# Kernel tuning notes

Measured on AMD Instinct MI355X. Metric: run time of the kernel, lower is better.

The kernel has to match this reference:

```python
import jax, jax.numpy as jnp
import numpy as np
from jax import lax

B, C, L = 32, 384, 3136
H_IMG = 56  # sqrt(L)
HEADS = 12
DH = C // HEADS
BN_EPS = 1e-5
ADD_EPS = 1e-12


def _branch(maps, dwk, g, b, pww, pwb, stride):
    # depthwise 3x3 conv, padding=1, no bias
    y = lax.conv_general_dilated(
        maps, dwk, window_strides=(stride, stride), padding=((1, 1), (1, 1)),
        dimension_numbers=("NCHW", "HWIO", "NCHW"), feature_group_count=C)
    # BatchNorm2d (training-mode batch stats, biased variance)
    mu = y.mean(axis=(0, 2, 3), keepdims=True)
    var = y.var(axis=(0, 2, 3), keepdims=True)
    y = (y - mu) * lax.rsqrt(var + BN_EPS)
    y = y * g[None, :, None, None] + b[None, :, None, None]
    # pointwise 1x1 conv with bias
    y = jnp.einsum("oc,bchw->bohw", pww, y) + pwb[None, :, None, None]
    return jax.nn.gelu(y, approximate=False)


def setup_inputs() -> dict:
    key = jax.random.key(0)
    ks = jax.random.split(key, 8)
    x = jax.random.normal(ks[0], (B, C, L), dtype=jnp.float32)
    dw_k = jax.random.normal(ks[1], (3, 3, 3, 1, C), dtype=jnp.float32) * 0.1  # [branch,kh,kw,1,C]
    bn2_g = jnp.ones((3, C), dtype=jnp.float32)
    bn2_b = jnp.zeros((3, C), dtype=jnp.float32)
    pw_w = jax.random.normal(ks[2], (3, C, C), dtype=jnp.float32) * (1.0 / np.sqrt(C))
    pw_b = jnp.zeros((3, C), dtype=jnp.float32)
    add_w = jnp.ones((2,), dtype=jnp.float32)
    bn1_g = jnp.ones((C,), dtype=jnp.float32)
    bn1_b = jnp.zeros((C,), dtype=jnp.float32)
    return {"x": x, "dw_k": dw_k, "bn2_g": bn2_g, "bn2_b": bn2_b,
            "pw_w": pw_w, "pw_b": pw_b, "add_w": add_w,
            "bn1_g": bn1_g, "bn1_b": bn1_b}


def reference(x, dw_k, bn2_g, bn2_b, pw_w, pw_b, add_w, bn1_g, bn1_b):
    b, c, l = x.shape
    maps = x.reshape(b, c, H_IMG, H_IMG)
    strides = (1, 2, 2)
    q, k, v = (_branch(maps, dw_k[i], bn2_g[i], bn2_b[i], pw_w[i], pw_b[i], strides[i])
               for i in range(3))
    # flatten spatial -> tokens: [B, Ltok, C] then split heads [B, Ltok, H, DH]
    def tok(t):
        bb, cc, hh, ww = t.shape
        return t.reshape(bb, cc, hh * ww).transpose(0, 2, 1).reshape(bb, hh * ww, HEADS, DH)
    qh, kh, vh = tok(q), tok(k), tok(v)
    qs = jax.nn.softmax(qh, axis=-1)      # softmax over per-head feature dim
    ks_ = jax.nn.softmax(kh, axis=1)      # softmax over k tokens
    kv = jnp.einsum("bkhd,bkhe->bhde", ks_, vh)      # [B, H, DH, DH]
    att = jnp.einsum("bqhd,bhde->bqhe", qs, kv)      # [B, Lq, H, DH]
    # per-head transpose(1,2) then cat along channels (head-major)
    att = att.transpose(0, 2, 3, 1).reshape(b, c, l)  # [B, C, L]
    # weighted residual add
    w = jax.nn.relu(add_w)
    wt = w / (w.sum() + ADD_EPS)
    y = wt[0] * att + wt[1] * x
    # BatchNorm1d over channels (training-mode batch stats)
    mu = y.mean(axis=(0, 2), keepdims=True)
    var = y.var(axis=(0, 2), keepdims=True)
    y = (y - mu) * lax.rsqrt(var + BN_EPS)
    return y * bn1_g[None, :, None] + bn1_b[None, :, None]
```

## Files before the change

kernel.cpp:

```cpp
#include <hip/hip_runtime.h>

typedef unsigned short u16;
typedef unsigned int u32;

#define NB 32
#define NC 384
#define NH 12
#define DHD 32
#define HI 56
#define LQ 3136
#define HO 28
#define LK 784

typedef _Float16 half8 __attribute__((ext_vector_type(8)));
typedef float f32x4 __attribute__((ext_vector_type(4)));

__device__ __forceinline__ u16 f2h(float f) {
  f = fminf(fmaxf(f, -60000.f), 60000.f);
  union { _Float16 h; u16 u; } v; v.h = (_Float16)f; return v.u;
}
__device__ __forceinline__ float h2f(u16 u) {
  union { u16 u; _Float16 h; } v; v.u = u; return (float)v.h;
}
__device__ __forceinline__ float gelu(float x) {
  return 0.5f * x * (1.0f + erff(x * 0.70710678118654752440f));
}

__global__ __launch_bounds__(256) void k_dwconv(
    const float* __restrict__ x, const float* __restrict__ dwk,
    u16* __restrict__ cq, u16* __restrict__ ck, u16* __restrict__ cv,
    float* __restrict__ stats2)
{
  const int c = blockIdx.x, b = blockIdx.y, t = threadIdx.x;
  __shared__ float pl[LQ];
  __shared__ float ker[32];
  __shared__ float redw[24];
  const float* xp = x + ((size_t)(b * NC + c)) * LQ;
  for (int i = t; i < LQ / 4; i += 256)
    ((float4*)pl)[i] = ((const float4*)xp)[i];
  if (t < 27) ker[t] = dwk[t * NC + c];
  __syncthreads();
  float s0 = 0, s1 = 0, s2 = 0, s3 = 0, s4 = 0, s5 = 0;
  u16* oq = cq + ((size_t)(b * NC + c)) * LQ;
  for (int p = t; p < LQ; p += 256) {
    const int h = p / HI, w = p - h * HI;
    float a = 0.f;
#pragma unroll
    for (int kh = 0; kh < 3; kh++) {
      const int hh = h + kh - 1;
      if (hh < 0 || hh >= HI) continue;
#pragma unroll
      for (int kw = 0; kw < 3; kw++) {
        const int ww = w + kw - 1;
        if (ww < 0 || ww >= HI) continue;
        a += ker[kh * 3 + kw] * pl[hh * HI + ww];
      }
    }
    const u16 rq = f2h(a);
    oq[p] = rq;
    const float ar = h2f(rq);
    s0 += ar; s1 += ar * ar;
  }
  u16* ok = ck + ((size_t)(b * NC + c)) * LK;
  u16* ov = cv + ((size_t)(b * NC + c)) * LK;
  for (int p = t; p < LK; p += 256) {
    const int h = p / HO, w = p - h * HO;
    float ak = 0.f, av = 0.f;
#pragma unroll
    for (int kh = 0; kh < 3; kh++) {
      const int hh = 2 * h + kh - 1;
      if (hh < 0 || hh >= HI) continue;
#pragma unroll
      for (int kw = 0; kw < 3; kw++) {
        const int ww = 2 * w + kw - 1;
        if (ww < 0 || ww >= HI) continue;
        const float xv = pl[hh * HI + ww];
        ak += ker[9 + kh * 3 + kw] * xv;
        av += ker[18 + kh * 3 + kw] * xv;
      }
    }
    const u16 rk = f2h(ak), rv = f2h(av);
    ok[p] = rk; ov[p] = rv;
    const float akr = h2f(rk), avr = h2f(rv);
    s2 += akr; s3 += akr * akr; s4 += avr; s5 += avr * avr;
  }
  const int lane = t & 63, wv = t >> 6;
#pragma unroll
  for (int off = 32; off > 0; off >>= 1) {
    s0 += __shfl_down(s0, off); s1 += __shfl_down(s1, off);
    s2 += __shfl_down(s2, off); s3 += __shfl_down(s3, off);
    s4 += __shfl_down(s4, off); s5 += __shfl_down(s5, off);
  }
  if (lane == 0) {
    redw[wv * 6 + 0] = s0; redw[wv * 6 + 1] = s1; redw[wv * 6 + 2] = s2;
    redw[wv * 6 + 3] = s3; redw[wv * 6 + 4] = s4; redw[wv * 6 + 5] = s5;
  }
  __syncthreads();
  if (t < 6) {
    const float tot = redw[t] + redw[6 + t] + redw[12 + t] + redw[18 + t];
    const int br = t >> 1, which = t & 1;
    atomicAdd(&stats2[((br * NC) + c) * 2 + which], tot);
  }
}

__global__ __launch_bounds__(128) void k_foldbn(
    const float* __restrict__ pww, const float* __restrict__ pwb,
    const float* __restrict__ g2, const float* __restrict__ b2,
    const float* __restrict__ stats2,
    u16* __restrict__ effw, float* __restrict__ effb)
{
  const int o = blockIdx.x, br = blockIdx.y, t = threadIdx.x;
  const float cnt = (br == 0) ? (float)(NB * LQ) : (float)(NB * LK);
  __shared__ float red[128];
  float bacc = 0.f;
  for (int c = t; c < NC; c += 128) {
    const float S = stats2[((br * NC) + c) * 2 + 0];
    const float S2 = stats2[((br * NC) + c) * 2 + 1];
    const float mu = S / cnt;
    const float var = fmaxf(S2 / cnt - mu * mu, 0.f);
    const float a = g2[br * NC + c] * rsqrtf(var + 1e-5f);
    const float bs = b2[br * NC + c] - mu * a;
    const size_t wi = (size_t)br * NC * NC + (size_t)o * NC + c;
    const float wvv = pww[wi];
    effw[wi] = f2h(wvv * a);
    bacc += wvv * bs;
  }
  red[t] = bacc;
  __syncthreads();
  for (int off = 64; off > 0; off >>= 1) {
    if (t < off) red[t] += red[t + off];
    __syncthreads();
  }
  if (t == 0) effb[br * NC + o] = red[0] + pwb[br * NC + o];
}

__global__ __launch_bounds__(256) void k_pwgemm(
    const u16* __restrict__ Y, const u16* __restrict__ W,
    const float* __restrict__ bias, u16* __restrict__ Out, const int N)
{
  const int nb = blockIdx.x * 128;
  const int mb = blockIdx.y * 128;
  const int b = blockIdx.z;
  const int t = threadIdx.x;
  const int lane = t & 63;
  const int wm = ((t >> 6) & 1) * 64, wn = ((t >> 6) >> 1) * 64;
  const int quad = lane >> 4, r16 = lane & 15;
  __shared__ u16 As[128 * 40];
  __shared__ u16 Bs[128 * 40];
  const u16* Yb = Y + (size_t)b * NC * N;
  f32x4 acc[4][4];
#pragma unroll
  for (int i = 0; i < 4; i++)
#pragma unroll
    for (int j = 0; j < 4; j++) acc[i][j] = (f32x4){0.f, 0.f, 0.f, 0.f};

  for (int k0 = 0; k0 < NC; k0 += 32) {
#pragma unroll
    for (int ld = 0; ld < 2; ld++) {
      const int cid = t + ld * 256;
      const int r = cid >> 2, q4 = cid & 3;
      const uint4 u = *(const uint4*)(W + (size_t)(mb + r) * NC + k0 + q4 * 8);
      *(uint4*)(&As[r * 40 + q4 * 8]) = u;
    }
    {
      const int kk2 = t >> 4;
      const int q4 = t & 15;
      const int n = nb + q4 * 8;
      union { uint4 u; u16 s[8]; } v0, v1;
      if (n < N) {
        const u16* yr0 = Yb + (size_t)(k0 + 2 * kk2) * N + n;
        v0.u = *(const uint4*)yr0;
        v1.u = *(const uint4*)(yr0 + N);
      } else {
        v0.u = make_uint4(0u, 0u, 0u, 0u);
        v1.u = make_uint4(0u, 0u, 0u, 0u);
      }
      const int col = (2 * kk2) ^ ((q4 & 3) << 3);
      u16* bp = &Bs[(q4 * 8) * 40 + col];
#pragma unroll
      for (int j = 0; j < 8; j++) {
        const u32 w = (u32)v0.s[j] | ((u32)v1.s[j] << 16);
        *(u32*)(bp + j * 40) = w;
      }
    }
    __syncthreads();
    half8 af[4], bfv[4];
#pragma unroll
    for (int sm = 0; sm < 4; sm++)
      af[sm] = *(const half8*)(&As[(wm + sm * 16 + r16) * 40 + quad * 8]);
#pragma unroll
    for (int sn = 0; sn < 4; sn++) {
      const int n = wn + sn * 16 + r16;
      bfv[sn] = *(const half8*)(&Bs[n * 40 + (((quad ^ (n >> 3)) & 3) << 3)]);
    }
#pragma unroll
    for (int sm = 0; sm < 4; sm++)
#pragma unroll
      for (int sn = 0; sn < 4; sn++)
        acc[sm][sn] = __builtin_amdgcn_mfma_f32_16x16x32_f16(af[sm], bfv[sn], acc[sm][sn], 0, 0, 0);
    __syncthreads();
  }
  u16* Ob = Out + (size_t)b * NC * N;
#pragma unroll
  for (int sm = 0; sm < 4; sm++) {
#pragma unroll
    for (int sn = 0; sn < 4; sn++) {
      const int n = nb + wn + sn * 16 + r16;
      if (n >= N) continue;
#pragma unroll
      for (int r = 0; r < 4; r++) {
        const int m = mb + wm + sm * 16 + quad * 4 + r;
        const float vv = gelu(acc[sm][sn][r] + bias[m]);
        Ob[(size_t)m * N + n] = f2h(vv);
      }
    }
  }
}

__global__ __launch_bounds__(256) void k_kv(
    const u16* __restrict__ kb_, const u16* __restrict__ vb_,
    float* __restrict__ kv)
{
  const int h = blockIdx.x, b = blockIdx.y;
  const int t = threadIdx.x, lane = t & 63, wv = t >> 6;
  __shared__ float mZ[64];
  __shared__ float ekt[128 * 33];
  __shared__ float vtt[128 * 33];
  const u16* kb = kb_ + ((size_t)(b * NC + h * DHD)) * LK;
  const u16* vb = vb_ + ((size_t)(b * NC + h * DHD)) * LK;
#pragma unroll
  for (int rr = 0; rr < 8; rr++) {
    const int d = wv * 8 + rr;
    const u16* row = kb + (size_t)d * LK;
    float mx = -1e30f;
    for (int l = lane; l < LK; l += 64) mx = fmaxf(mx, h2f(row[l]));
#pragma unroll
    for (int off = 32; off > 0; off >>= 1) mx = fmaxf(mx, __shfl_xor(mx, off));
    float se = 0.f;
    for (int l = lane; l < LK; l += 64) se += __expf(h2f(row[l]) - mx);
#pragma unroll
    for (int off = 32; off > 0; off >>= 1) se += __shfl_xor(se, off);
    if (lane == 0) { mZ[d] = mx; mZ[32 + d] = se; }
  }
  __syncthreads();
  const int d = t >> 3, e4 = (t & 7) * 4;
  float a0 = 0, a1 = 0, a2 = 0, a3 = 0;
  const int rr = t >> 3;
  const int ls = (t & 7) * 16;
  const u16* krow = kb + (size_t)rr * LK;
  const u16* vrow = vb + (size_t)rr * LK;
  const float mrow = mZ[rr];
  for (int l0 = 0; l0 < LK; l0 += 128) {
#pragma unroll
    for (int j = 0; j < 16; j++) {
      const int l = l0 + ls + j;
      const bool ok = l < LK;
      ekt[(ls + j) * 33 + rr] = ok ? __expf(h2f(krow[l]) - mrow) : 0.f;
      vtt[(ls + j) * 33 + rr] = ok ? h2f(vrow[l]) : 0.f;
    }
    __syncthreads();
    for (int lc = 0; lc < 128; lc++) {
      const float kd = ekt[lc * 33 + d];
      a0 += kd * vtt[lc * 33 + e4 + 0];
      a1 += kd * vtt[lc * 33 + e4 + 1];
      a2 += kd * vtt[lc * 33 + e4 + 2];
      a3 += kd * vtt[lc * 33 + e4 + 3];
    }
    __syncthreads();
  }
  const float rz = 1.0f / mZ[32 + d];
  float* kvp = kv + ((size_t)(b * NH + h) * DHD + d) * DHD + e4;
  kvp[0] = a0 * rz; kvp[1] = a1 * rz; kvp[2] = a2 * rz; kvp[3] = a3 * rz;
}

__global__ __launch_bounds__(256) void k_att(
    u16* __restrict__ qy, const float* __restrict__ x,
    const float* __restrict__ kv, const float* __restrict__ addw,
    float* __restrict__ stats1)
{
  const int chunk = blockIdx.x, h = blockIdx.y, b = blockIdx.z;
  const int t = threadIdx.x;
  __shared__ float kvs[DHD * DHD];
  __shared__ float2 st16[4][DHD][17];
  __shared__ float wred[4][64];
  const float* kvp = kv + (size_t)(b * NH + h) * (DHD * DHD);
  for (int i = t; i < DHD * DHD; i += 256) kvs[i] = kvp[i];
  float w0 = fmaxf(addw[0], 0.f);
  float w1 = fmaxf(addw[1], 0.f);
  const float wsum = w0 + w1 + 1e-12f;
  w0 /= wsum; w1 /= wsum;
  __syncthreads();
  const int l0 = chunk * 512 + 2 * t;
  const bool valid = (l0 + 1) < LQ;
  const int lc = valid ? l0 : 0;
  u16* qp = qy + ((size_t)(b * NC + h * DHD)) * LQ + lc;
  const float* xp = x + ((size_t)(b * NC + h * DHD)) * LQ + lc;

  float acc0[DHD], acc1[DHD];
#pragma unroll
  for (int e = 0; e < DHD; e++) { acc0[e] = 0.f; acc1[e] = 0.f; }

  if (valid) {
    float p0[DHD], p1[DHD];
    float mx0 = -1e30f, mx1 = -1e30f;
#pragma unroll
    for (int d = 0; d < DHD; d++) {
      const u32 u = *(const u32*)(qp + (size_t)d * LQ);
      p0[d] = h2f((u16)(u & 0xffffu));
      p1[d] = h2f((u16)(u >> 16));
      mx0 = fmaxf(mx0, p0[d]); mx1 = fmaxf(mx1, p1[d]);
    }
    float se0 = 0.f, se1 = 0.f;
#pragma unroll
    for (int d = 0; d < DHD; d++) {
      p0[d] = __expf(p0[d] - mx0); se0 += p0[d];
      p1[d] = __expf(p1[d] - mx1); se1 += p1[d];
    }
    const float rs0 = 1.0f / se0, rs1 = 1.0f / se1;
    for (int d = 0; d < DHD; d++) {
      const float s0 = p0[d] * rs0, s1 = p1[d] * rs1;
      const float* kr = &kvs[d * DHD];
#pragma unroll
      for (int e = 0; e < DHD; e++) {
        const float kd = kr[e];
        acc0[e] += s0 * kd; acc1[e] += s1 * kd;
      }
    }
  }

  const int lane = t & 63, wv = t >> 6;
#pragma unroll
  for (int e = 0; e < DHD; e++) {
    float v0 = 0.f, v1 = 0.f;
    if (valid) {
      const float2 xv = *(const float2*)(xp + (size_t)e * LQ);
      const float y0 = w0 * acc0[e] + w1 * xv.x;
      const float y1 = w0 * acc1[e] + w1 * xv.y;
      const u16 r0 = f2h(y0), r1 = f2h(y1);
      *(u32*)(qp + (size_t)e * LQ) = (u32)r0 | ((u32)r1 << 16);
      v0 = h2f(r0); v1 = h2f(r1);
    }
    float s = v0 + v1, q = v0 * v0 + v1 * v1;
    s += __shfl_down(s, 32); q += __shfl_down(q, 32);
    s += __shfl_down(s, 16); q += __shfl_down(q, 16);
    if (lane < 16) st16[wv][e][lane] = make_float2(s, q);
  }
  {
    const int col = t >> 1;
    const int wvs = col >> 5;
    const int es = col & 31;
    const int half = t & 1;
    float s = 0.f, q = 0.f;
#pragma unroll
    for (int i = 0; i < 8; i++) {
      const float2 v = st16[wvs][es][half * 8 + i];
      s += v.x; q += v.y;
    }
    s += __shfl_down(s, 1); q += __shfl_down(q, 1);
    if (half == 0) { wred[wvs][es] = s; wred[wvs][32 + es] = q; }
  }
  __syncthreads();
  if (t < 64) {
    const float tot = wred[0][t] + wred[1][t] + wred[2][t] + wred[3][t];
    const int e = t & 31, which = t >> 5;
    atomicAdd(&stats1[(h * DHD + e) * 2 + which], tot);
  }
}

__global__ void k_bn1coef(const float* __restrict__ stats1,
                          const float* __restrict__ g1, const float* __restrict__ b1,
                          float* __restrict__ ss)
{
  const int c = threadIdx.x;
  if (c >= NC) return;
  const float cnt = (float)NB * (float)LQ;
  const float S = stats1[c * 2], S2 = stats1[c * 2 + 1];
  const float mu = S / cnt;
  const float var = fmaxf(S2 / cnt - mu * mu, 0.f);
  const float a = g1[c] * rsqrtf(var + 1e-5f);
  ss[c * 2] = a;
  ss[c * 2 + 1] = b1[c] - mu * a;
}

__global__ __launch_bounds__(256) void k_bn1apply(
    const u16* __restrict__ ybuf, const float* __restrict__ ss, float* __restrict__ out)
{
  const int c = blockIdx.x, b = blockIdx.y, t = threadIdx.x;
  const float a = ss[c * 2], sh = ss[c * 2 + 1];
  const uint4* yp = (const uint4*)(ybuf + ((size_t)(b * NC + c)) * LQ);
  float4* op = (float4*)(out + ((size_t)(b * NC + c)) * LQ);
  for (int i = t; i < LQ / 8; i += 256) {
    union { uint4 u; u16 us[8]; } v;
    v.u = yp[i];
    float4 o0, o1;
    o0.x = a * h2f(v.us[0]) + sh; o0.y = a * h2f(v.us[1]) + sh;
    o0.z = a * h2f(v.us[2]) + sh; o0.w = a * h2f(v.us[3]) + sh;
    o1.x = a * h2f(v.us[4]) + sh; o1.y = a * h2f(v.us[5]) + sh;
    o1.z = a * h2f(v.us[6]) + sh; o1.w = a * h2f(v.us[7]) + sh;
    op[i * 2] = o0; op[i * 2 + 1] = o1;
  }
}

extern "C" void kernel_launch(void* const* d_in, const int* in_sizes, int n_in,
                              void* d_out, int out_size, void* d_ws, size_t ws_size,
                              hipStream_t stream)
{
  const float* x    = (const float*)d_in[0];
  const float* dwk  = (const float*)d_in[1];
  const float* g2   = (const float*)d_in[2];
  const float* b2   = (const float*)d_in[3];
  const float* pww  = (const float*)d_in[4];
  const float* pwb  = (const float*)d_in[5];
  const float* addw = (const float*)d_in[6];
  const float* g1   = (const float*)d_in[7];
  const float* b1   = (const float*)d_in[8];
  float* out = (float*)d_out;

  const size_t SQ = (size_t)NB * NC * LQ;
  const size_t SK = (size_t)NB * NC * LK;

  float* stats2 = (float*)d_ws;
  float* stats1 = stats2 + 3 * NC * 2;
  float* ss     = stats1 + NC * 2;
  float* effb   = ss + NC * 2;
  float* kv     = effb + 3 * NC;
  u16* effw     = (u16*)(kv + (size_t)NB * NH * DHD * DHD);
  u16* convq    = effw + (size_t)3 * NC * NC;
  u16* qbuf     = convq + SQ;
  u16* convk    = qbuf;
  u16* convv    = qbuf + SK;
  u16* kbuf     = qbuf + 2 * SK;
  u16* vbuf     = convk;

  hipMemsetAsync(stats2, 0, (3 * NC * 2 + NC * 2) * sizeof(float), stream);

  k_dwconv<<<dim3(NC, NB), 256, 0, stream>>>(x, dwk, convq, convk, convv, stats2);
  k_foldbn<<<dim3(NC, 3), 128, 0, stream>>>(pww, pwb, g2, b2, stats2, effw, effb);
  k_pwgemm<<<dim3(7, 3, NB), 256, 0, stream>>>(convk, effw + (size_t)1 * NC * NC, effb + NC, kbuf, LK);
  k_pwgemm<<<dim3(7, 3, NB), 256, 0, stream>>>(convv, effw + (size_t)2 * NC * NC, effb + 2 * NC, vbuf, LK);
  k_kv<<<dim3(NH, NB), 256, 0, stream>>>(kbuf, vbuf, kv);
  k_pwgemm<<<dim3(25, 3, NB), 256, 0, stream>>>(convq, effw, effb, qbuf, LQ);
  k_att<<<dim3(7, NH, NB), 256, 0, stream>>>(qbuf, x, kv, addw, stats1);
  k_bn1coef<<<1, NC, 0, stream>>>(stats1, g1, b1, ss);
  k_bn1apply<<<dim3(NC, NB), 256, 0, stream>>>(qbuf, ss, out);
}
```

Measured before the change: 762.2 us.

## Fuse Q pointwise GEMM with attention epilogue in one kernel

Merges the Q-branch pointwise GEMM (with GELU) and the attention/residual/stat kernel. The Q tile now stays in shared memory in a swizzled layout, so the fp16 Q tensor is no longer written to and read back from global memory. Each 128x128 tile covers four heads, one wave per head, and each lane handles two tokens. The cost is about 66KB of shared memory per block, which lowers occupancy. The softmax/kv part now runs with only 64 tokens per wave per block, so the per-block epilogue work is heavier.

```diff
diff --git a/kernel.cpp b/kernel.cpp
--- a/kernel.cpp
+++ b/kernel.cpp
@@ -273,28 +273,119 @@
   kvp[0] = a0 * rz; kvp[1] = a1 * rz; kvp[2] = a2 * rz; kvp[3] = a3 * rz;
 }
 
-__global__ __launch_bounds__(256) void k_att(
-    u16* __restrict__ qy, const float* __restrict__ x,
-    const float* __restrict__ kv, const float* __restrict__ addw,
-    float* __restrict__ stats1)
-{
-  const int chunk = blockIdx.x, h = blockIdx.y, b = blockIdx.z;
+__global__ __launch_bounds__(256) void k_qatt(
+    const u16* __restrict__ Yq, const u16* __restrict__ W,
+    const float* __restrict__ bias, const float* __restrict__ x,
+    const float* __restrict__ kvg, const float* __restrict__ addw,
+    u16* __restrict__ ybuf, float* __restrict__ stats1)
+{
+  __shared__ __align__(16) char smem[67584];
+  u16* As = (u16*)smem;
+  u16* Bs = (u16*)(smem + 10240);
+  u32* qs32 = (u32*)smem;
+  float* kvs = (float*)(smem + 32768);
+  float2* st = (float2*)(smem + 49152);
+  float* wred = (float*)(smem + 66560);
+
+  const int nb = blockIdx.x * 128;
+  const int mb = blockIdx.y * 128;
+  const int b = blockIdx.z;
   const int t = threadIdx.x;
-  __shared__ float kvs[DHD * DHD];
-  __shared__ float2 st16[4][DHD][17];
-  __shared__ float wred[4][64];
-  const float* kvp = kv + (size_t)(b * NH + h) * (DHD * DHD);
-  for (int i = t; i < DHD * DHD; i += 256) kvs[i] = kvp[i];
+  const int lane = t & 63, wv = t >> 6;
+  const int wm = ((t >> 6) & 1) * 64, wn = ((t >> 6) >> 1) * 64;
+  const int quad = lane >> 4, r16 = lane & 15;
+
+  {
+    const float* src = kvg + ((size_t)(b * NH) + blockIdx.y * 4) * (DHD * DHD);
+    for (int i = t; i < (4 * DHD * DHD) / 4; i += 256)
+      ((float4*)kvs)[i] = ((const float4*)src)[i];
+  }
   float w0 = fmaxf(addw[0], 0.f);
   float w1 = fmaxf(addw[1], 0.f);
   const float wsum = w0 + w1 + 1e-12f;
   w0 /= wsum; w1 /= wsum;
+
+  const u16* Yb = Yq + (size_t)b * NC * LQ;
+  f32x4 acc[4][4];
+#pragma unroll
+  for (int i = 0; i < 4; i++)
+#pragma unroll
+    for (int j = 0; j < 4; j++) acc[i][j] = (f32x4){0.f, 0.f, 0.f, 0.f};
+
+  for (int k0 = 0; k0 < NC; k0 += 32) {
+#pragma unroll
+    for (int ld = 0; ld < 2; ld++) {
+      const int cid = t + ld * 256;
+      const int r = cid >> 2, q4 = cid & 3;
+      const uint4 u = *(const uint4*)(W + (size_t)(mb + r) * NC + k0 + q4 * 8);
+      *(uint4*)(&As[r * 40 + q4 * 8]) = u;
+    }
+    {
+      const int kk2 = t >> 4;
+      const int q4 = t & 15;
+      const int n = nb + q4 * 8;
+      union { uint4 u; u16 s[8]; } v0, v1;
+      if (n < LQ) {
+        const u16* yr0 = Yb + (size_t)(k0 + 2 * kk2) * LQ + n;
+        v0.u = *(const uint4*)yr0;
+        v1.u = *(const uint4*)(yr0 + LQ);
+      } else {
+        v0.u = make_uint4(0u, 0u, 0u, 0u);
+        v1.u = make_uint4(0u, 0u, 0u, 0u);
+      }
+      const int col = (2 * kk2) ^ ((q4 & 3) << 3);
+      u16* bp = &Bs[(q4 * 8) * 40 + col];
+#pragma unroll
+      for (int j = 0; j < 8; j++) {
+        const u32 w = (u32)v0.s[j] | ((u32)v1.s[j] << 16);
+        *(u32*)(bp + j * 40) = w;
+      }
+    }
+    __syncthreads();
+    half8 af[4], bfv[4];
+#pragma unroll
+    for (int sm = 0; sm < 4; sm++)
+      af[sm] = *(const half8*)(&As[(wm + sm * 16 + r16) * 40 + quad * 8]);
+#pragma unroll
+    for (int sn = 0; sn < 4; sn++) {
+      const int n = wn + sn * 16 + r16;
+      bfv[sn] = *(const half8*)(&Bs[n * 40 + (((quad ^ (n >> 3)) & 3) << 3)]);
+    }
+#pragma unroll
+    for (int sm = 0; sm < 4; sm++)
+#pragma unroll
+      for (int sn = 0; sn < 4; sn++)
+        acc[sm][sn] = __builtin_amdgcn_mfma_f32_16x16x32_f16(af[sm], bfv[sn], acc[sm][sn], 0, 0, 0);
+    __syncthreads();
+  }
+
+#pragma unroll
+  for (int sm = 0; sm < 4; sm++) {
+#pragma unroll
+    for (int sn = 0; sn < 4; sn++) {
+      const int tokl = wn + sn * 16 + r16;
+#pragma unroll
+      for (int r = 0; r < 4; r++) {
+        const int ch = wm + sm * 16 + quad * 4 + r;
+        const u32 qv = (u32)f2h(gelu(acc[sm][sn][r] + bias[mb + ch]));
+        const u32 qo = (u32)__shfl_xor((int)qv, 1);
+        if (!(r16 & 1)) {
+          const int dcol = ((tokl >> 1) ^ ((ch & 31) << 1)) & 63;
+          qs32[ch * 64 + dcol] = qv | (qo << 16);
+        }
+      }
+    }
+  }
   __syncthreads();
-  const int l0 = chunk * 512 + 2 * t;
-  const bool valid = (l0 + 1) < LQ;
-  const int lc = valid ? l0 : 0;
-  u16* qp = qy + ((size_t)(b * NC + h * DHD)) * LQ + lc;
-  const float* xp = x + ((size_t)(b * NC + h * DHD)) * LQ + lc;
+
+  const int hloc = wv;
+  const int hg = blockIdx.y * 4 + hloc;
+  const int tp = lane;
+  const int tok0 = nb + 2 * tp;
+  const bool valid = (tok0 + 1) < LQ;
+  const int lc = valid ? tok0 : 0;
+  const float* xp = x + ((size_t)(b * NC + hg * DHD)) * LQ + lc;
+  u16* yp = ybuf + ((size_t)(b * NC + hg * DHD)) * LQ + lc;
 
   float acc0[DHD], acc1[DHD];
 #pragma unroll
@@ -305,7 +396,7 @@
     float mx0 = -1e30f, mx1 = -1e30f;
 #pragma unroll
     for (int d = 0; d < DHD; d++) {
-      const u32 u = *(const u32*)(qp + (size_t)d * LQ);
+      const u32 u = qs32[(hloc * 32 + d) * 64 + ((tp ^ (d << 1)) & 63)];
       p0[d] = h2f((u16)(u & 0xffffu));
       p1[d] = h2f((u16)(u >> 16));
       mx0 = fmaxf(mx0, p0[d]); mx1 = fmaxf(mx1, p1[d]);
@@ -319,7 +410,7 @@
     const float rs0 = 1.0f / se0, rs1 = 1.0f / se1;
     for (int d = 0; d < DHD; d++) {
       const float s0 = p0[d] * rs0, s1 = p1[d] * rs1;
-      const float* kr = &kvs[d * DHD];
+      const float* kr = kvs + hloc * (DHD * DHD) + d * DHD;
 #pragma unroll
       for (int e = 0; e < DHD; e++) {
         const float kd = kr[e];
@@ -328,7 +419,6 @@
     }
   }
 
-  const int lane = t & 63, wv = t >> 6;
 #pragma unroll
   for (int e = 0; e < DHD; e++) {
     float v0 = 0.f, v1 = 0.f;
@@ -337,13 +427,13 @@
       const float y0 = w0 * acc0[e] + w1 * xv.x;
       const float y1 = w0 * acc1[e] + w1 * xv.y;
       const u16 r0 = f2h(y0), r1 = f2h(y1);
-      *(u32*)(qp + (size_t)e * LQ) = (u32)r0 | ((u32)r1 << 16);
+      *(u32*)(yp + (size_t)e * LQ) = (u32)r0 | ((u32)r1 << 16);
       v0 = h2f(r0); v1 = h2f(r1);
     }
     float s = v0 + v1, q = v0 * v0 + v1 * v1;
     s += __shfl_down(s, 32); q += __shfl_down(q, 32);
     s += __shfl_down(s, 16); q += __shfl_down(q, 16);
-    if (lane < 16) st16[wv][e][lane] = make_float2(s, q);
+    if (lane < 16) st[(wv * 32 + e) * 17 + lane] = make_float2(s, q);
   }
   {
     const int col = t >> 1;
@@ -353,17 +443,16 @@
     float s = 0.f, q = 0.f;
 #pragma unroll
     for (int i = 0; i < 8; i++) {
-      const float2 v = st16[wvs][es][half * 8 + i];
+      const float2 v = st[(wvs * 32 + es) * 17 + half * 8 + i];
       s += v.x; q += v.y;
     }
     s += __shfl_down(s, 1); q += __shfl_down(q, 1);
-    if (half == 0) { wred[wvs][es] = s; wred[wvs][32 + es] = q; }
-  }
-  __syncthreads();
-  if (t < 64) {
-    const float tot = wred[0][t] + wred[1][t] + wred[2][t] + wred[3][t];
-    const int e = t & 31, which = t >> 5;
-    atomicAdd(&stats1[(h * DHD + e) * 2 + which], tot);
+    if (half == 0) { wred[wvs * 64 + es] = s; wred[wvs * 64 + 32 + es] = q; }
+  }
+  {
+    const float val = wred[wv * 64 + lane];
+    const int e = lane & 31, which = lane >> 5;
+    atomicAdd(&stats1[(hg * DHD + e) * 2 + which], val);
   }
 }
 
@@ -426,10 +515,10 @@
   float* kv     = effb + 3 * NC;
   u16* effw     = (u16*)(kv + (size_t)NB * NH * DHD * DHD);
   u16* convq    = effw + (size_t)3 * NC * NC;
-  u16* qbuf     = convq + SQ;
-  u16* convk    = qbuf;
-  u16* convv    = qbuf + SK;
-  u16* kbuf     = qbuf + 2 * SK;
+  u16* ybuf     = convq + SQ;
+  u16* convk    = ybuf;
+  u16* convv    = ybuf + SK;
+  u16* kbuf     = ybuf + 2 * SK;
   u16* vbuf     = convk;
 
   hipMemsetAsync(stats2, 0, (3 * NC * 2 + NC * 2) * sizeof(float), stream);
@@ -439,8 +528,7 @@
   k_pwgemm<<<dim3(7, 3, NB), 256, 0, stream>>>(convk, effw + (size_t)1 * NC * NC, effb + NC, kbuf, LK);
   k_pwgemm<<<dim3(7, 3, NB), 256, 0, stream>>>(convv, effw + (size_t)2 * NC * NC, effb + 2 * NC, vbuf, LK);
   k_kv<<<dim3(NH, NB), 256, 0, stream>>>(kbuf, vbuf, kv);
-  k_pwgemm<<<dim3(25, 3, NB), 256, 0, stream>>>(convq, effw, effb, qbuf, LQ);
-  k_att<<<dim3(7, NH, NB), 256, 0, stream>>>(qbuf, x, kv, addw, stats1);
+  k_qatt<<<dim3(25, 3, NB), 256, 0, stream>>>(convq, effw, effb, x, kv, addw, ybuf, stats1);
   k_bn1coef<<<1, NC, 0, stream>>>(stats1, g1, b1, ss);
-  k_bn1apply<<<dim3(NC, NB), 256, 0, stream>>>(qbuf, ss, out);
-}
+  k_bn1apply<<<dim3(NC, NB), 256, 0, stream>>>(ybuf, ss, out);
+}
```

Measured after the change: 808.9 us. +6.1%, slower.
